# Performance work log

Hardware: AMD Instinct MI355X
Metric: run time of the kernel (lower is better)

## Reference

```python
import jax, jax.numpy as jnp
import numpy as np

FEAT = 1024   # feat_dim
EMB = 64      # emb_dim
GROUP = 16    # group == fc_dim
DG = FEAT // GROUP  # 64, per-group query/key dim and conv out channels per group
R = 1024      # num_rois
N = 1024      # nongt_dim


def setup_inputs() -> dict:
    key = jax.random.key(0)
    ks = jax.random.split(key, 8)
    inp = {
        "position_embedding": jax.random.normal(ks[0], (R, N, EMB), dtype=jnp.float32),
        "roi_feat": jax.random.normal(ks[1], (R, FEAT), dtype=jnp.float32),
        # fc_q / fc_k: Linear(feat_dim, feat_dim)
        "Wq": jax.random.normal(ks[2], (FEAT, FEAT), dtype=jnp.float32) * 0.02,
        "bq": jnp.zeros((FEAT,), dtype=jnp.float32),
        "Wk": jax.random.normal(ks[3], (FEAT, FEAT), dtype=jnp.float32) * 0.02,
        "bk": jnp.zeros((FEAT,), dtype=jnp.float32),
        # fc_pos_feat: Linear(emb_dim, fc_dim=group)
        "Wp": jax.random.normal(ks[4], (GROUP, EMB), dtype=jnp.float32) * 0.1,
        "bp": jnp.zeros((GROUP,), dtype=jnp.float32),
        # conv_cat: Conv2d(group*feat_dim, feat_dim, k=1, groups=group)
        # per group g: in FEAT channels -> out DG channels. Shape [GROUP, DG, FEAT].
        "Wc": jax.random.normal(ks[5], (GROUP, DG, FEAT), dtype=jnp.float32) * 0.02,
        "bc": jnp.zeros((FEAT,), dtype=jnp.float32),
        "nongt_dim": N,
    }
    return inp


def reference(position_embedding, roi_feat, Wq, bq, Wk, bk, Wp, bp, Wc, bc, nongt_dim):
    scale = 1.0 / np.sqrt(float(DG))
    # fc_pos_feat + relu -> aff_weight [R, GROUP, N]
    pos_feat = jax.nn.relu(jnp.einsum("rne,ge->rng", position_embedding, Wp) + bp)
    aff_weight = jnp.transpose(pos_feat, (0, 2, 1))  # [R, GROUP, N]
    nongt = roi_feat[:nongt_dim]                     # [N, FEAT]
    q = (roi_feat @ Wq.T + bq).reshape(-1, GROUP, DG)   # [R, GROUP, DG]
    k = (nongt @ Wk.T + bk).reshape(-1, GROUP, DG)      # [N, GROUP, DG]
    # per-group QK^T with log position bias
    aff = jnp.einsum("rgd,ngd->rgn", q, k) * scale      # [R, GROUP, N]
    weighted = jnp.log(jnp.clip(aff_weight, 1e-6, None)) + aff
    att = jax.nn.softmax(weighted, axis=2)              # [R, GROUP, N]
    # attention * V -> [R, GROUP, FEAT]
    out_t = jnp.einsum("rgn,nf->rgf", att, nongt)
    # grouped 1x1 conv combine: group g maps FEAT -> DG output channels
    out = jnp.einsum("rgf,gof->rgo", out_t, Wc).reshape(-1, FEAT) + bc
    return out
```

## Files before the change

kernel.cpp:

```cpp
#include <hip/hip_runtime.h>

#define R_DIM 1024
#define N_DIM 1024
#define FEAT  1024
#define EMB   64
#define GROUP 16
#define DG    64

typedef _Float16 half8  __attribute__((ext_vector_type(8)));
typedef _Float16 half4v __attribute__((ext_vector_type(4)));
typedef float    f32x4  __attribute__((ext_vector_type(4)));

__device__ __forceinline__ half8 cvt8(const float* p) {
  const float4 a = *(const float4*)p;
  const float4 b = *(const float4*)(p + 4);
  half8 h;
  h[0] = (_Float16)a.x; h[1] = (_Float16)a.y; h[2] = (_Float16)a.z; h[3] = (_Float16)a.w;
  h[4] = (_Float16)b.x; h[5] = (_Float16)b.y; h[6] = (_Float16)b.z; h[7] = (_Float16)b.w;
  return h;
}

__global__ __launch_bounds__(256) void qk_gemm(
    const float* __restrict__ roi, const float* __restrict__ Wq,
    const float* __restrict__ bq,  const float* __restrict__ Wk,
    const float* __restrict__ bk,  _Float16* __restrict__ qh,
    _Float16* __restrict__ kh)
{
  __shared__ float aT[16][68];
  __shared__ float bqT[16][68];
  __shared__ float bkT[16][68];
  const int t  = threadIdx.x;
  const int r0 = blockIdx.x * 64, c0 = blockIdx.y * 64;
  const int lr = t >> 2, lk = (t & 3) << 2;
  const int ty = t >> 4, tx = t & 15;
  const float* ap  = roi + (r0 + lr) * FEAT + lk;
  const float* bqp = Wq  + (c0 + lr) * FEAT + lk;
  const float* bkp = Wk  + (c0 + lr) * FEAT + lk;
  float4 av  = *(const float4*)ap;
  float4 bqv = *(const float4*)bqp;
  float4 bkv = *(const float4*)bkp;
  float accq[4][4] = {}, acck[4][4] = {};
  for (int k0 = 0; k0 < FEAT; k0 += 16) {
    aT[lk+0][lr]=av.x;   aT[lk+1][lr]=av.y;   aT[lk+2][lr]=av.z;   aT[lk+3][lr]=av.w;
    bqT[lk+0][lr]=bqv.x; bqT[lk+1][lr]=bqv.y; bqT[lk+2][lr]=bqv.z; bqT[lk+3][lr]=bqv.w;
    bkT[lk+0][lr]=bkv.x; bkT[lk+1][lr]=bkv.y; bkT[lk+2][lr]=bkv.z; bkT[lk+3][lr]=bkv.w;
    __syncthreads();
    const bool more = (k0 + 16) < FEAT;
    float4 av_n, bqv_n, bkv_n;
    if (more) {
      av_n  = *(const float4*)(ap  + k0 + 16);
      bqv_n = *(const float4*)(bqp + k0 + 16);
      bkv_n = *(const float4*)(bkp + k0 + 16);
    }
#pragma unroll
    for (int kk = 0; kk < 16; ++kk) {
      const float4 a4 = *(const float4*)&aT[kk][ty << 2];
      const float4 q4 = *(const float4*)&bqT[kk][tx << 2];
      const float4 k4 = *(const float4*)&bkT[kk][tx << 2];
      const float ar[4] = {a4.x, a4.y, a4.z, a4.w};
      const float qr[4] = {q4.x, q4.y, q4.z, q4.w};
      const float kr[4] = {k4.x, k4.y, k4.z, k4.w};
#pragma unroll
      for (int i = 0; i < 4; ++i)
#pragma unroll
        for (int j = 0; j < 4; ++j) {
          accq[i][j] += ar[i] * qr[j];
          acck[i][j] += ar[i] * kr[j];
        }
    }
    __syncthreads();
    if (more) { av = av_n; bqv = bqv_n; bkv = bkv_n; }
  }
  const float4 bq4 = *(const float4*)(bq + c0 + (tx << 2));
  const float4 bk4 = *(const float4*)(bk + c0 + (tx << 2));
  const float bqr[4] = {bq4.x, bq4.y, bq4.z, bq4.w};
  const float bkr[4] = {bk4.x, bk4.y, bk4.z, bk4.w};
#pragma unroll
  for (int i = 0; i < 4; ++i) {
    half4v oq, ok;
#pragma unroll
    for (int j = 0; j < 4; ++j) {
      oq[j] = (_Float16)(accq[i][j] + bqr[j]);
      ok[j] = (_Float16)(acck[i][j] + bkr[j]);
    }
    const int row = r0 + (ty << 2) + i;
    *(half4v*)(qh + (size_t)row * FEAT + c0 + (tx << 2)) = oq;
    *(half4v*)(kh + (size_t)row * FEAT + c0 + (tx << 2)) = ok;
  }
}

__global__ __launch_bounds__(256) void pos_mfma(
    const float* __restrict__ pe, const float* __restrict__ Wp,
    const float* __restrict__ bp, _Float16* __restrict__ logw)
{
  __shared__ __align__(16) _Float16 Xs[128 * 64];
  __shared__ __align__(16) _Float16 LW[16][136];
  const int t  = threadIdx.x;
  const int bx = blockIdx.x;
  const int r  = bx >> 3;
  const int n0 = (bx & 7) << 7;
  const size_t gbase = ((size_t)bx << 13);

#pragma unroll
  for (int i = 0; i < 8; ++i) {
    const int flat4 = (i << 8) + t;
    const int row = flat4 >> 4, e4 = flat4 & 15;
    const float4 v = *(const float4*)(pe + gbase + ((size_t)flat4 << 2));
    half4v h;
    h[0] = (_Float16)v.x; h[1] = (_Float16)v.y;
    h[2] = (_Float16)v.z; h[3] = (_Float16)v.w;
    const int boff = (row << 7) + (((e4 << 3)) ^ ((row & 7) << 4));
    *(half4v*)((char*)Xs + boff) = h;
  }

  const int w = t >> 6, l = t & 63, q16 = l & 15, q4 = l >> 4;
  const float* wpp = Wp + (q16 << 6) + (q4 << 3);
  const half8 wb0 = cvt8(wpp);
  const half8 wb1 = cvt8(wpp + 32);
  const float bpg = bp[q16];
  __syncthreads();

#pragma unroll
  for (int tt = 0; tt < 2; ++tt) {
    const int lrbase = (w << 5) + (tt << 4);
    const int lr = lrbase + q16;
    const int b0 = (lr << 7) + (((q4 << 4))      ^ ((lr & 7) << 4));
    const int b1 = (lr << 7) + (((q4 << 4) + 64) ^ ((lr & 7) << 4));
    const half8 a0 = *(const half8*)((const char*)Xs + b0);
    const half8 a1 = *(const half8*)((const char*)Xs + b1);
    f32x4 acc = (f32x4){0.f, 0.f, 0.f, 0.f};
    acc = __builtin_amdgcn_mfma_f32_16x16x32_f16(a0, wb0, acc, 0, 0, 0);
    acc = __builtin_amdgcn_mfma_f32_16x16x32_f16(a1, wb1, acc, 0, 0, 0);
    half4v o;
#pragma unroll
    for (int j = 0; j < 4; ++j) {
      const float v = fmaxf(acc[j] + bpg, 1e-6f);
      o[j] = (_Float16)__logf(v);
    }
    *(half4v*)&LW[q16][lrbase + (q4 << 2)] = o;
  }
  __syncthreads();

  const int g = t >> 4, n4 = t & 15;
  const half8 vv = *(const half8*)&LW[g][n4 << 3];
  *(half8*)(logw + ((size_t)((r << 4) + g) << 10) + n0 + (n4 << 3)) = vv;
}

__global__ __launch_bounds__(256) void kc_gemm(
    const float* __restrict__ roi, const float* __restrict__ Wc,
    _Float16* __restrict__ kct)
{
  __shared__ float aT[16][68];
  __shared__ float bT[16][68];
  const int t  = threadIdx.x;
  const int n0 = blockIdx.x * 64;
  const int g  = blockIdx.y;
  const int lr = t >> 2, lk = (t & 3) << 2;
  const int ty = t >> 4, tx = t & 15;
  const float* ap  = Wc  + (size_t)(g * DG + lr) * FEAT + lk;
  const float* bp_ = roi + (size_t)(n0 + lr) * FEAT + lk;
  float4 av = *(const float4*)ap;
  float4 bv = *(const float4*)bp_;
  float acc[4][4] = {};
  for (int k0 = 0; k0 < FEAT; k0 += 16) {
    aT[lk+0][lr]=av.x; aT[lk+1][lr]=av.y; aT[lk+2][lr]=av.z; aT[lk+3][lr]=av.w;
    bT[lk+0][lr]=bv.x; bT[lk+1][lr]=bv.y; bT[lk+2][lr]=bv.z; bT[lk+3][lr]=bv.w;
    __syncthreads();
    const bool more = (k0 + 16) < FEAT;
    float4 av_n, bv_n;
    if (more) {
      av_n = *(const float4*)(ap  + k0 + 16);
      bv_n = *(const float4*)(bp_ + k0 + 16);
    }
#pragma unroll
    for (int kk = 0; kk < 16; ++kk) {
      const float4 a4 = *(const float4*)&aT[kk][ty << 2];
      const float4 b4 = *(const float4*)&bT[kk][tx << 2];
      const float ar[4] = {a4.x, a4.y, a4.z, a4.w};
      const float br[4] = {b4.x, b4.y, b4.z, b4.w};
#pragma unroll
      for (int i = 0; i < 4; ++i)
#pragma unroll
        for (int j = 0; j < 4; ++j) acc[i][j] += ar[i] * br[j];
    }
    __syncthreads();
    if (more) { av = av_n; bv = bv_n; }
  }
#pragma unroll
  for (int i = 0; i < 4; ++i) {
    half4v o4;
#pragma unroll
    for (int j = 0; j < 4; ++j) o4[j] = (_Float16)acc[i][j];
    *(half4v*)(kct + (size_t)((g << 6) + (ty << 2) + i) * N_DIM + n0 + (tx << 2)) = o4;
  }
}

#define PLD 1032
__global__ __launch_bounds__(256) void attn_mfma(
    const _Float16* __restrict__ qh, const _Float16* __restrict__ kh,
    const _Float16* __restrict__ logw, const _Float16* __restrict__ kct,
    const float* __restrict__ bc, float* __restrict__ outp)
{
  __shared__ __align__(16) _Float16 P[16][PLD];
  __shared__ float Ored[4][16][68];
  __shared__ float redm[4][16];
  __shared__ float redl[4][16];

  const int t   = threadIdx.x;
  const int w   = t >> 6;
  const int l   = t & 63;
  const int q16 = l & 15;
  const int q4  = l >> 4;
  const int g   = blockIdx.y;
  const int r0  = blockIdx.x << 4;
  const int nbase = w << 8;

  const half8* qp = (const half8*)(qh + (size_t)(r0 + q16) * FEAT + (g << 6) + (q4 << 3));
  const half8 a0 = qp[0];
  const half8 a1 = qp[4];

  f32x4 S[16];
#pragma unroll
  for (int i = 0; i < 16; ++i) S[i] = (f32x4){0.f, 0.f, 0.f, 0.f};
#pragma unroll
  for (int t16 = 0; t16 < 16; ++t16) {
    const int n0 = nbase + (t16 << 4);
    const half8* kp = (const half8*)(kh + (size_t)(n0 + q16) * FEAT + (g << 6) + (q4 << 3));
    S[t16] = __builtin_amdgcn_mfma_f32_16x16x32_f16(a0, kp[0], S[t16], 0, 0, 0);
    S[t16] = __builtin_amdgcn_mfma_f32_16x16x32_f16(a1, kp[4], S[t16], 0, 0, 0);
  }

#pragma unroll
  for (int t16 = 0; t16 < 16; ++t16) {
    const int n = nbase + (t16 << 4) + q16;
#pragma unroll
    for (int j = 0; j < 4; ++j) {
      const int r = r0 + (q4 << 2) + j;
      const float lw = (float)logw[(size_t)(((r << 4) + g) << 10) + n];
      S[t16][j] = S[t16][j] * 0.125f + lw;
    }
  }

  float m[4] = {-1e30f, -1e30f, -1e30f, -1e30f};
#pragma unroll
  for (int t16 = 0; t16 < 16; ++t16)
#pragma unroll
    for (int j = 0; j < 4; ++j) m[j] = fmaxf(m[j], S[t16][j]);
#pragma unroll
  for (int off = 8; off; off >>= 1)
#pragma unroll
    for (int j = 0; j < 4; ++j) m[j] = fmaxf(m[j], __shfl_xor(m[j], off));
  if (q16 == 0) {
#pragma unroll
    for (int j = 0; j < 4; ++j) redm[w][(q4 << 2) + j] = m[j];
  }
  __syncthreads();
#pragma unroll
  for (int j = 0; j < 4; ++j) {
    const int r = (q4 << 2) + j;
    m[j] = fmaxf(fmaxf(redm[0][r], redm[1][r]), fmaxf(redm[2][r], redm[3][r]));
  }

  float ls[4] = {0.f, 0.f, 0.f, 0.f};
#pragma unroll
  for (int t16 = 0; t16 < 16; ++t16) {
    const int n = nbase + (t16 << 4) + q16;
#pragma unroll
    for (int j = 0; j < 4; ++j) {
      const float p = __expf(S[t16][j] - m[j]);
      ls[j] += p;
      P[(q4 << 2) + j][n] = (_Float16)p;
    }
  }
#pragma unroll
  for (int off = 8; off; off >>= 1)
#pragma unroll
    for (int j = 0; j < 4; ++j) ls[j] += __shfl_xor(ls[j], off);
  if (q16 == 0) {
#pragma unroll
    for (int j = 0; j < 4; ++j) redl[w][(q4 << 2) + j] = ls[j];
  }
  __syncthreads();

  f32x4 O[4];
#pragma unroll
  for (int ot = 0; ot < 4; ++ot) O[ot] = (f32x4){0.f, 0.f, 0.f, 0.f};
#pragma unroll
  for (int ks = 0; ks < 8; ++ks) {
    const int nk = nbase + (ks << 5) + (q4 << 3);
    const half8 pa = *(const half8*)&P[q16][nk];
#pragma unroll
    for (int ot = 0; ot < 4; ++ot) {
      const half8 bfr = *(const half8*)(kct + (size_t)((g << 6) + (ot << 4) + q16) * N_DIM + nk);
      O[ot] = __builtin_amdgcn_mfma_f32_16x16x32_f16(pa, bfr, O[ot], 0, 0, 0);
    }
  }
#pragma unroll
  for (int ot = 0; ot < 4; ++ot)
#pragma unroll
    for (int j = 0; j < 4; ++j)
      Ored[w][(q4 << 2) + j][(ot << 4) + q16] = O[ot][j];
  __syncthreads();

  const int r  = t >> 4;
  const int o0 = (t & 15) << 2;
  const float lsum = redl[0][r] + redl[1][r] + redl[2][r] + redl[3][r];
  const float inv  = 1.0f / lsum;
  float o[4];
#pragma unroll
  for (int c = 0; c < 4; ++c)
    o[c] = Ored[0][r][o0 + c] + Ored[1][r][o0 + c] + Ored[2][r][o0 + c] + Ored[3][r][o0 + c];
  const float4 bcv = *(const float4*)(bc + (g << 6) + o0);
  float4 res;
  res.x = o[0] * inv + bcv.x;
  res.y = o[1] * inv + bcv.y;
  res.z = o[2] * inv + bcv.z;
  res.w = o[3] * inv + bcv.w;
  *(float4*)(outp + (size_t)(r0 + r) * FEAT + (g << 6) + o0) = res;
}

extern "C" void kernel_launch(void* const* d_in, const int* in_sizes, int n_in,
                              void* d_out, int out_size, void* d_ws, size_t ws_size,
                              hipStream_t stream)
{
  const float* pe  = (const float*)d_in[0];
  const float* roi = (const float*)d_in[1];
  const float* Wq  = (const float*)d_in[2];
  const float* bq  = (const float*)d_in[3];
  const float* Wk  = (const float*)d_in[4];
  const float* bk  = (const float*)d_in[5];
  const float* Wp  = (const float*)d_in[6];
  const float* bp  = (const float*)d_in[7];
  const float* Wc  = (const float*)d_in[8];
  const float* bc  = (const float*)d_in[9];
  float* outp = (float*)d_out;

  char* ws = (char*)d_ws;
  _Float16* qh   = (_Float16*)(ws);
  _Float16* kh   = (_Float16*)(ws + ((size_t)2 << 20));
  _Float16* kct  = (_Float16*)(ws + ((size_t)4 << 20));
  _Float16* logw = (_Float16*)(ws + ((size_t)6 << 20));

  qk_gemm<<<dim3(16, 16), 256, 0, stream>>>(roi, Wq, bq, Wk, bk, qh, kh);
  pos_mfma<<<8192, 256, 0, stream>>>(pe, Wp, bp, logw);
  kc_gemm<<<dim3(16, 16), 256, 0, stream>>>(roi, Wc, kct);
  attn_mfma<<<dim3(64, 16), 256, 0, stream>>>(qh, kh, logw, kct, bc, outp);
}
```

Measured before the change: 201.8 us.

## Interleave K and Wc·roi layouts, persist pos blocks with prefetch, remap attention grid

K and the Wc-projected values are written in a group-major interleaved layout (8-element chunks contiguous across rows), so the attention kernel's MFMA operand loads become contiguous per group instead of strided by FEAT or N. The position-embedding kernel now processes four row blocks per workgroup and prefetches the next tile into registers while computing the current one, cutting the grid to a quarter. The attention launch becomes 1D with a block-to-(group,row) mapping that keeps neighbouring blocks on the same groups for L2 reuse. The cost is higher register pressure from the prefetch buffers and more complex indexing.

```diff
diff --git a/kernel.cpp b/kernel.cpp
--- a/kernel.cpp
+++ b/kernel.cpp
@@ -24,7 +24,7 @@
     const float* __restrict__ roi, const float* __restrict__ Wq,
     const float* __restrict__ bq,  const float* __restrict__ Wk,
     const float* __restrict__ bk,  _Float16* __restrict__ qh,
-    _Float16* __restrict__ kh)
+    _Float16* __restrict__ khI)
 {
   __shared__ float aT[16][68];
   __shared__ float bqT[16][68];
@@ -75,6 +75,7 @@
   const float4 bk4 = *(const float4*)(bk + c0 + (tx << 2));
   const float bqr[4] = {bq4.x, bq4.y, bq4.z, bq4.w};
   const float bkr[4] = {bk4.x, bk4.y, bk4.z, bk4.w};
+  const int g  = c0 >> 6;
 #pragma unroll
   for (int i = 0; i < 4; ++i) {
     half4v oq, ok;
@@ -85,7 +86,7 @@
     }
     const int row = r0 + (ty << 2) + i;
     *(half4v*)(qh + (size_t)row * FEAT + c0 + (tx << 2)) = oq;
-    *(half4v*)(kh + (size_t)row * FEAT + c0 + (tx << 2)) = ok;
+    *(half4v*)(khI + ((((size_t)g << 3) + (tx >> 1)) << 13) + (row << 3) + ((tx & 1) << 2)) = ok;
   }
 }
 
@@ -97,68 +98,81 @@
   __shared__ __align__(16) _Float16 LW[16][136];
   const int t  = threadIdx.x;
   const int bx = blockIdx.x;
-  const int r  = bx >> 3;
-  const int n0 = (bx & 7) << 7;
-  const size_t gbase = ((size_t)bx << 13);
-
-#pragma unroll
-  for (int i = 0; i < 8; ++i) {
-    const int flat4 = (i << 8) + t;
-    const int row = flat4 >> 4, e4 = flat4 & 15;
-    const float4 v = *(const float4*)(pe + gbase + ((size_t)flat4 << 2));
-    half4v h;
-    h[0] = (_Float16)v.x; h[1] = (_Float16)v.y;
-    h[2] = (_Float16)v.z; h[3] = (_Float16)v.w;
-    const int boff = (row << 7) + (((e4 << 3)) ^ ((row & 7) << 4));
-    *(half4v*)((char*)Xs + boff) = h;
-  }
-
   const int w = t >> 6, l = t & 63, q16 = l & 15, q4 = l >> 4;
+
   const float* wpp = Wp + (q16 << 6) + (q4 << 3);
   const half8 wb0 = cvt8(wpp);
   const half8 wb1 = cvt8(wpp + 32);
   const float bpg = bp[q16];
-  __syncthreads();
-
-#pragma unroll
-  for (int tt = 0; tt < 2; ++tt) {
-    const int lrbase = (w << 5) + (tt << 4);
-    const int lr = lrbase + q16;
-    const int b0 = (lr << 7) + (((q4 << 4))      ^ ((lr & 7) << 4));
-    const int b1 = (lr << 7) + (((q4 << 4) + 64) ^ ((lr & 7) << 4));
-    const half8 a0 = *(const half8*)((const char*)Xs + b0);
-    const half8 a1 = *(const half8*)((const char*)Xs + b1);
-    f32x4 acc = (f32x4){0.f, 0.f, 0.f, 0.f};
-    acc = __builtin_amdgcn_mfma_f32_16x16x32_f16(a0, wb0, acc, 0, 0, 0);
-    acc = __builtin_amdgcn_mfma_f32_16x16x32_f16(a1, wb1, acc, 0, 0, 0);
-    half4v o;
-#pragma unroll
-    for (int j = 0; j < 4; ++j) {
-      const float v = fmaxf(acc[j] + bpg, 1e-6f);
-      o[j] = (_Float16)__logf(v);
-    }
-    *(half4v*)&LW[q16][lrbase + (q4 << 2)] = o;
-  }
-  __syncthreads();
-
-  const int g = t >> 4, n4 = t & 15;
-  const half8 vv = *(const half8*)&LW[g][n4 << 3];
-  *(half8*)(logw + ((size_t)((r << 4) + g) << 10) + n0 + (n4 << 3)) = vv;
+
+  const size_t base = ((size_t)bx) << 15;
+  float4 cur[8], nxt[8];
+#pragma unroll
+  for (int i = 0; i < 8; ++i)
+    cur[i] = *(const float4*)(pe + base + ((size_t)((i << 8) + t) << 2));
+
+  for (int tt = 0; tt < 4; ++tt) {
+    if (tt < 3) {
+#pragma unroll
+      for (int i = 0; i < 8; ++i)
+        nxt[i] = *(const float4*)(pe + base + ((size_t)(((tt + 1) << 11) + (i << 8) + t) << 2));
+    }
+#pragma unroll
+    for (int i = 0; i < 8; ++i) {
+      const int flat4 = (i << 8) + t;
+      const int row = flat4 >> 4, e4 = flat4 & 15;
+      half4v h;
+      h[0] = (_Float16)cur[i].x; h[1] = (_Float16)cur[i].y;
+      h[2] = (_Float16)cur[i].z; h[3] = (_Float16)cur[i].w;
+      const int boff = (row << 7) + ((e4 << 3) ^ ((row & 7) << 4));
+      *(half4v*)((char*)Xs + boff) = h;
+    }
+    __syncthreads();
+#pragma unroll
+    for (int sub = 0; sub < 2; ++sub) {
+      const int lrbase = (w << 5) + (sub << 4);
+      const int lrr = lrbase + q16;
+      const int b0 = (lrr << 7) + (((q4 << 4))      ^ ((lrr & 7) << 4));
+      const int b1 = (lrr << 7) + (((q4 << 4) + 64) ^ ((lrr & 7) << 4));
+      const half8 a0 = *(const half8*)((const char*)Xs + b0);
+      const half8 a1 = *(const half8*)((const char*)Xs + b1);
+      f32x4 acc = (f32x4){0.f, 0.f, 0.f, 0.f};
+      acc = __builtin_amdgcn_mfma_f32_16x16x32_f16(a0, wb0, acc, 0, 0, 0);
+      acc = __builtin_amdgcn_mfma_f32_16x16x32_f16(a1, wb1, acc, 0, 0, 0);
+      half4v o;
+#pragma unroll
+      for (int j = 0; j < 4; ++j) {
+        const float v = fmaxf(acc[j] + bpg, 1e-6f);
+        o[j] = (_Float16)__logf(v);
+      }
+      *(half4v*)&LW[q16][lrbase + (q4 << 2)] = o;
+    }
+    __syncthreads();
+    const int rowblk = (bx << 2) + tt;
+    const int r = rowblk >> 3, n0 = (rowblk & 7) << 7;
+    const int gg = t >> 4, n4 = t & 15;
+    const half8 vv = *(const half8*)&LW[gg][n4 << 3];
+    *(half8*)(logw + ((size_t)((r << 4) + gg) << 10) + n0 + (n4 << 3)) = vv;
+    if (tt < 3) {
+#pragma unroll
+      for (int i = 0; i < 8; ++i) cur[i] = nxt[i];
+    }
+  }
 }
 
 __global__ __launch_bounds__(256) void kc_gemm(
     const float* __restrict__ roi, const float* __restrict__ Wc,
-    _Float16* __restrict__ kct)
+    _Float16* __restrict__ kctI)
 {
   __shared__ float aT[16][68];
   __shared__ float bT[16][68];
-  const int t  = threadIdx.x;
-  const int n0 = blockIdx.x * 64;
-  const int g  = blockIdx.y;
+  const int t   = threadIdx.x;
+  const int n0g = blockIdx.x * 64;
+  const int g   = blockIdx.y;
   const int lr = t >> 2, lk = (t & 3) << 2;
   const int ty = t >> 4, tx = t & 15;
   const float* ap  = Wc  + (size_t)(g * DG + lr) * FEAT + lk;
-  const float* bp_ = roi + (size_t)(n0 + lr) * FEAT + lk;
+  const float* bp_ = roi + (size_t)(n0g + lr) * FEAT + lk;
   float4 av = *(const float4*)ap;
   float4 bv = *(const float4*)bp_;
   float acc[4][4] = {};
@@ -191,43 +205,49 @@
     half4v o4;
 #pragma unroll
     for (int j = 0; j < 4; ++j) o4[j] = (_Float16)acc[i][j];
-    *(half4v*)(kct + (size_t)((g << 6) + (ty << 2) + i) * N_DIM + n0 + (tx << 2)) = o4;
-  }
-}
-
-#define PLD 1032
+    *(half4v*)(kctI + ((((size_t)g << 7) + ((n0g + (tx << 2)) >> 3)) << 9)
+               + (((ty << 2) + i) << 3) + ((tx & 1) << 2)) = o4;
+  }
+}
+
 __global__ __launch_bounds__(256) void attn_mfma(
-    const _Float16* __restrict__ qh, const _Float16* __restrict__ kh,
-    const _Float16* __restrict__ logw, const _Float16* __restrict__ kct,
+    const _Float16* __restrict__ qh, const _Float16* __restrict__ khI,
+    const _Float16* __restrict__ logw, const _Float16* __restrict__ kctI,
     const float* __restrict__ bc, float* __restrict__ outp)
 {
-  __shared__ __align__(16) _Float16 P[16][PLD];
   __shared__ float Ored[4][16][68];
   __shared__ float redm[4][16];
   __shared__ float redl[4][16];
+#define PLD 1032
+  __shared__ __align__(16) _Float16 P[16][PLD];
 
   const int t   = threadIdx.x;
   const int w   = t >> 6;
   const int l   = t & 63;
   const int q16 = l & 15;
   const int q4  = l >> 4;
-  const int g   = blockIdx.y;
-  const int r0  = blockIdx.x << 4;
+  const int bid = blockIdx.x;
+  const int g   = (bid & 7) + ((bid >> 9) << 3);
+  const int r0  = ((bid >> 3) & 63) << 4;
   const int nbase = w << 8;
 
   const half8* qp = (const half8*)(qh + (size_t)(r0 + q16) * FEAT + (g << 6) + (q4 << 3));
   const half8 a0 = qp[0];
   const half8 a1 = qp[4];
 
+  const _Float16* kbase = khI  + ((size_t)g << 16);
+  const _Float16* cbase = kctI + ((size_t)g << 16);
+
   f32x4 S[16];
 #pragma unroll
   for (int i = 0; i < 16; ++i) S[i] = (f32x4){0.f, 0.f, 0.f, 0.f};
 #pragma unroll
   for (int t16 = 0; t16 < 16; ++t16) {
-    const int n0 = nbase + (t16 << 4);
-    const half8* kp = (const half8*)(kh + (size_t)(n0 + q16) * FEAT + (g << 6) + (q4 << 3));
-    S[t16] = __builtin_amdgcn_mfma_f32_16x16x32_f16(a0, kp[0], S[t16], 0, 0, 0);
-    S[t16] = __builtin_amdgcn_mfma_f32_16x16x32_f16(a1, kp[4], S[t16], 0, 0, 0);
+    const int n = nbase + (t16 << 4) + q16;
+    const half8 k0 = *(const half8*)(kbase + ((size_t)q4 << 13) + (n << 3));
+    const half8 k1 = *(const half8*)(kbase + ((size_t)(4 + q4) << 13) + (n << 3));
+    S[t16] = __builtin_amdgcn_mfma_f32_16x16x32_f16(a0, k0, S[t16], 0, 0, 0);
+    S[t16] = __builtin_amdgcn_mfma_f32_16x16x32_f16(a1, k1, S[t16], 0, 0, 0);
   }
 
 #pragma unroll
@@ -291,7 +311,7 @@
     const half8 pa = *(const half8*)&P[q16][nk];
 #pragma unroll
     for (int ot = 0; ot < 4; ++ot) {
-      const half8 bfr = *(const half8*)(kct + (size_t)((g << 6) + (ot << 4) + q16) * N_DIM + nk);
+      const half8 bfr = *(const half8*)(cbase + ((size_t)(nk >> 3) << 9) + (((ot << 4) + q16) << 3));
       O[ot] = __builtin_amdgcn_mfma_f32_16x16x32_f16(pa, bfr, O[ot], 0, 0, 0);
     }
   }
@@ -337,12 +357,12 @@
 
   char* ws = (char*)d_ws;
   _Float16* qh   = (_Float16*)(ws);
-  _Float16* kh   = (_Float16*)(ws + ((size_t)2 << 20));
-  _Float16* kct  = (_Float16*)(ws + ((size_t)4 << 20));
+  _Float16* khI  = (_Float16*)(ws + ((size_t)2 << 20));
+  _Float16* kctI = (_Float16*)(ws + ((size_t)4 << 20));
   _Float16* logw = (_Float16*)(ws + ((size_t)6 << 20));
 
-  qk_gemm<<<dim3(16, 16), 256, 0, stream>>>(roi, Wq, bq, Wk, bk, qh, kh);
-  pos_mfma<<<8192, 256, 0, stream>>>(pe, Wp, bp, logw);
-  kc_gemm<<<dim3(16, 16), 256, 0, stream>>>(roi, Wc, kct);
-  attn_mfma<<<dim3(64, 16), 256, 0, stream>>>(qh, kh, logw, kct, bc, outp);
-}
+  qk_gemm<<<dim3(16, 16), 256, 0, stream>>>(roi, Wq, bq, Wk, bk, qh, khI);
+  pos_mfma<<<2048, 256, 0, stream>>>(pe, Wp, bp, logw);
+  kc_gemm<<<dim3(16, 16), 256, 0, stream>>>(roi, Wc, kctI);
+  attn_mfma<<<1024, 256, 0, stream>>>(qh, khI, logw, kctI, bc, outp);
+}
```

Measured after the change: 190.4 us. 5.6% less time.
